# Optimization experiments

Measured on AMD Instinct MI355X. Metric: run time of the kernel, lower is better.

The kernel has to match this reference:

```python
import jax, jax.numpy as jnp
import numpy as np

IN_FEATURES = 4096
OUT_FEATURES = 768
N_BITS = 8
SCALE = float(2 ** N_BITS - 1)  # 255
REG_WEIGHT = 0.001


def setup_inputs() -> dict:
    key = jax.random.key(0)
    k1, k2, k3 = jax.random.split(key, 3)
    latent = jax.random.normal(k1, (1024, IN_FEATURES), dtype=jnp.float32)
    true_sum = jax.random.uniform(k2, (1024, OUT_FEATURES * N_BITS), dtype=jnp.float32)
    # nn.init.uniform_(weight, -0.1, 0.1)
    weight = jax.random.uniform(k3, (IN_FEATURES, OUT_FEATURES * N_BITS),
                                dtype=jnp.float32, minval=-0.1, maxval=0.1)
    return {"latent": latent, "true_sum": true_sum, "weight": weight}


def _powers():
    # [1, 2, 4, ..., 2^(n-1)] with the top (sign) bit negated -> two's complement
    p = 2.0 ** jnp.arange(N_BITS, dtype=jnp.float32)
    return p.at[-1].multiply(-1.0)


def reference(latent, true_sum, weight):
    prob_weights = jax.nn.sigmoid(weight)                      # [in, out*n_bits]
    # min(|p-0|, |p-1|) = min(p, 1-p) for p in (0,1)
    reg_loss = REG_WEIGHT * jnp.minimum(prob_weights, 1.0 - prob_weights).mean()

    powers = _powers()                                         # [n_bits]
    int_weights = jnp.einsum('iob,b->io',
                             prob_weights.reshape(IN_FEATURES, -1, N_BITS),
                             powers)                           # [in, out]
    int_sum = jnp.einsum('nob,b->no',
                         true_sum.reshape(true_sum.shape[0], -1, N_BITS),
                         powers)                               # [B, out]

    # (latent[:, :, None] * int_weights[None]).sum(-2) == latent @ int_weights
    pred = jnp.einsum('bi,io->bo', latent, int_weights)        # [B, out]

    recon_loss = jnp.mean((pred / SCALE - int_sum / SCALE) ** 2)
    return (recon_loss + reg_loss, recon_loss, reg_loss)
```

## Files before the change

### kernel.cpp

```cpp
#include <hip/hip_runtime.h>
#include <hip/hip_bf16.h>
#include <stdint.h>

#define IN_F   4096
#define OUT_F  768
#define OUTB   (OUT_F * 8)
#define BATCH  1024
#define SPLITK 4
#define KSPAN  (IN_F / SPLITK)
#define BK     64
#define NIT    (KSPAN / BK)
#define PLANE  (BATCH * OUT_F)
#define PLANE4 (PLANE / 4)
#define EPIBLK 768

typedef short short8  __attribute__((ext_vector_type(8)));
typedef float f32x4   __attribute__((ext_vector_type(4)));
typedef unsigned int u32;

#define WS_WP    12582912
#define WS_LABF  18874368
#define WS_REGP  27262976
#define WS_SQP   27269120

__device__ __forceinline__ ushort f2bf(float f) {
    uint32_t u = __builtin_bit_cast(uint32_t, f);
    u += 0x7FFFu + ((u >> 16) & 1u);
    return (ushort)(u >> 16);
}

__device__ __forceinline__ float waveReduceSum(float v) {
    #pragma unroll
    for (int off = 32; off > 0; off >>= 1) v += __shfl_down(v, off, 64);
    return v;
}

__device__ __forceinline__ void glds16(const void* g, void* l) {
    __builtin_amdgcn_global_load_lds(
        (const __attribute__((address_space(1))) u32*)g,
        (__attribute__((address_space(3))) u32*)l, 16, 0, 0);
}

__global__ __launch_bounds__(256) void k_weights(const float* __restrict__ w,
                                                 const float* __restrict__ latent,
                                                 ushort* __restrict__ wp,
                                                 ushort* __restrict__ labf,
                                                 float* __restrict__ regpart) {
    if (blockIdx.x >= 1536) {
        int t = (blockIdx.x - 1536) * 256 + threadIdx.x;
        const float4* src = (const float4*)latent;
        uint4* dst = (uint4*)labf;
        #pragma unroll
        for (int j = 0; j < 4; j++) {
            int o = j * 131072 + t;
            float4 a0 = src[2 * o];
            float4 a1 = src[2 * o + 1];
            union { ushort u[8]; uint4 v; } pk;
            pk.u[0] = f2bf(a0.x); pk.u[1] = f2bf(a0.y); pk.u[2] = f2bf(a0.z); pk.u[3] = f2bf(a0.w);
            pk.u[4] = f2bf(a1.x); pk.u[5] = f2bf(a1.y); pk.u[6] = f2bf(a1.z); pk.u[7] = f2bf(a1.w);
            dst[o] = pk.v;
        }
        return;
    }

    int t  = blockIdx.x * 256 + threadIdx.x;
    int o  = t % OUT_F;
    int i8 = t / OUT_F;
    const float* src = w + (size_t)(i8 * 8) * OUTB + (size_t)o * 8;

    const float P[8] = {1.f, 2.f, 4.f, 8.f, 16.f, 32.f, 64.f, -128.f};
    float regsum = 0.f;
    union { ushort u[8]; uint4 v; } pk;

    #pragma unroll
    for (int r = 0; r < 8; r++) {
        float4 a = *(const float4*)(src + (size_t)r * OUTB);
        float4 b = *(const float4*)(src + (size_t)r * OUTB + 4);
        float x[8] = {a.x, a.y, a.z, a.w, b.x, b.y, b.z, b.w};
        float iw = 0.f;
        #pragma unroll
        for (int j = 0; j < 8; j++) {
            float p = __builtin_amdgcn_rcpf(1.f + __expf(-x[j]));
            iw += p * P[j];
            regsum += fminf(p, 1.f - p);
        }
        pk.u[r] = f2bf(iw);
    }
    *(uint4*)(wp + ((size_t)i8 * OUT_F + o) * 8) = pk.v;

    float ws = waveReduceSum(regsum);
    __shared__ float red[4];
    int lane = threadIdx.x & 63, wv = threadIdx.x >> 6;
    if (lane == 0) red[wv] = ws;
    __syncthreads();
    if (threadIdx.x == 0) regpart[blockIdx.x] = red[0] + red[1] + red[2] + red[3];
}

__global__ __launch_bounds__(256) void k_gemm(const ushort* __restrict__ labf,
                                              const ushort* __restrict__ wp,
                                              float* __restrict__ predp) {
    __shared__ __align__(16) ushort lA[2][64 * 72];
    __shared__ __align__(16) ushort lB[2][8 * 1032];

    const int tid  = threadIdx.x;
    const int n0   = blockIdx.x * 64;
    const int m0   = blockIdx.y * 64;
    const int bz   = blockIdx.z;
    const int kbase = bz * KSPAN;
    const int kg0   = kbase >> 3;
    const int lane = tid & 63, w = tid >> 6;
    const int wm = w >> 1, wn = w & 1;
    const int quad = lane >> 4, l16 = lane & 15;

    f32x4 acc[2][2] = {{{0.f,0.f,0.f,0.f},{0.f,0.f,0.f,0.f}},
                       {{0.f,0.f,0.f,0.f},{0.f,0.f,0.f,0.f}}};

    const int ar = tid >> 2, ac = tid & 3;
    const ushort* aptr = labf + (size_t)(m0 + ar) * IN_F + kbase + ac * 16;
    const ushort* bbase = wp + ((size_t)kg0 * OUT_F + n0 + lane) * 8;

    int buf = 0;
    glds16(bbase + (size_t)(2 * w) * OUT_F * 8,     &lB[0][(2 * w) * 1032]);
    glds16(bbase + (size_t)(2 * w + 1) * OUT_F * 8, &lB[0][(2 * w + 1) * 1032]);
    {
        uint4 a0 = *(const uint4*)aptr;
        uint4 a1 = *(const uint4*)(aptr + 8);
        *(uint4*)&lA[0][ar * 72 + ac * 16]     = a0;
        *(uint4*)&lA[0][ar * 72 + ac * 16 + 8] = a1;
    }
    __syncthreads();

    for (int it = 0; it < NIT; ++it) {
        const int nxt = buf ^ 1;
        uint4 a0, a1;
        if (it + 1 < NIT) {
            const ushort* bp = bbase + (size_t)(it + 1) * 8 * OUT_F * 8;
            glds16(bp + (size_t)(2 * w) * OUT_F * 8,     &lB[nxt][(2 * w) * 1032]);
            glds16(bp + (size_t)(2 * w + 1) * OUT_F * 8, &lB[nxt][(2 * w + 1) * 1032]);
            a0 = *(const uint4*)(aptr + (it + 1) * BK);
            a1 = *(const uint4*)(aptr + (it + 1) * BK + 8);
        }
        #pragma unroll
        for (int s = 0; s < 2; ++s) {
            short8 af0 = *(short8*)&lA[buf][(wm * 32 + l16) * 72 + s * 32 + quad * 8];
            short8 af1 = *(short8*)&lA[buf][(wm * 32 + 16 + l16) * 72 + s * 32 + quad * 8];
            short8 bf0 = *(short8*)&lB[buf][(s * 4 + quad) * 1032 + (wn * 32 + l16) * 8];
            short8 bf1 = *(short8*)&lB[buf][(s * 4 + quad) * 1032 + (wn * 32 + 16 + l16) * 8];
            acc[0][0] = __builtin_amdgcn_mfma_f32_16x16x32_bf16(af0, bf0, acc[0][0], 0, 0, 0);
            acc[0][1] = __builtin_amdgcn_mfma_f32_16x16x32_bf16(af0, bf1, acc[0][1], 0, 0, 0);
            acc[1][0] = __builtin_amdgcn_mfma_f32_16x16x32_bf16(af1, bf0, acc[1][0], 0, 0, 0);
            acc[1][1] = __builtin_amdgcn_mfma_f32_16x16x32_bf16(af1, bf1, acc[1][1], 0, 0, 0);
        }
        if (it + 1 < NIT) {
            *(uint4*)&lA[nxt][ar * 72 + ac * 16]     = a0;
            *(uint4*)&lA[nxt][ar * 72 + ac * 16 + 8] = a1;
        }
        __syncthreads();
        buf = nxt;
    }

    float* plane = predp + (size_t)bz * PLANE;
    #pragma unroll
    for (int fm = 0; fm < 2; fm++)
    #pragma unroll
    for (int fn = 0; fn < 2; fn++)
    #pragma unroll
    for (int r = 0; r < 4; r++) {
        int m = m0 + wm * 32 + fm * 16 + quad * 4 + r;
        int n = n0 + wn * 32 + fn * 16 + l16;
        plane[(size_t)m * OUT_F + n] = acc[fm][fn][r];
    }
}

__global__ __launch_bounds__(256) void k_epi(const float* __restrict__ predp,
                                             const float* __restrict__ tsum,
                                             float* __restrict__ sqpart) {
    int g = blockIdx.x * 256 + threadIdx.x;
    int m = g / (OUT_F / 4);
    int c = g % (OUT_F / 4);
    const float4* pp = (const float4*)predp;
    float4 p0 = pp[g];
    float4 p1 = pp[g + PLANE4];
    float4 p2 = pp[g + 2 * PLANE4];
    float4 p3 = pp[g + 3 * PLANE4];
    float pv[4] = {p0.x + p1.x + p2.x + p3.x, p0.y + p1.y + p2.y + p3.y,
                   p0.z + p1.z + p2.z + p3.z, p0.w + p1.w + p2.w + p3.w};
    const float* ts = tsum + (size_t)m * OUTB + (size_t)c * 32;
    float lsum = 0.f;
    #pragma unroll
    for (int j = 0; j < 4; j++) {
        float4 t0 = *(const float4*)(ts + j * 8);
        float4 t1 = *(const float4*)(ts + j * 8 + 4);
        float isum = t0.x + 2.f * t0.y + 4.f * t0.z + 8.f * t0.w
                   + 16.f * t1.x + 32.f * t1.y + 64.f * t1.z - 128.f * t1.w;
        float d = pv[j] - isum;
        lsum += d * d;
    }
    float wsum = waveReduceSum(lsum);
    __shared__ float red[4];
    if ((threadIdx.x & 63) == 0) red[threadIdx.x >> 6] = wsum;
    __syncthreads();
    if (threadIdx.x == 0)
        sqpart[blockIdx.x] = red[0] + red[1] + red[2] + red[3];
}

__global__ __launch_bounds__(256) void k_fin(const float* __restrict__ regpart,
                                             const float* __restrict__ sqpart,
                                             float* __restrict__ out) {
    int tid = threadIdx.x;
    float r = 0.f, s = 0.f;
    #pragma unroll
    for (int j = 0; j < 6; j++) r += regpart[tid + j * 256];
    #pragma unroll
    for (int j = 0; j < 3; j++) s += sqpart[tid + j * 256];
    r = waveReduceSum(r);
    s = waveReduceSum(s);
    __shared__ float redR[4], redS[4];
    int lane = tid & 63, wv = tid >> 6;
    if (lane == 0) { redR[wv] = r; redS[wv] = s; }
    __syncthreads();
    if (tid == 0) {
        float R = redR[0] + redR[1] + redR[2] + redR[3];
        float S = redS[0] + redS[1] + redS[2] + redS[3];
        float recon = S / ((float)(BATCH * OUT_F) * 255.f * 255.f);
        float reg   = 0.001f * R / (float)((size_t)IN_F * OUTB);
        out[0] = recon + reg;
        out[1] = recon;
        out[2] = reg;
    }
}

extern "C" void kernel_launch(void* const* d_in, const int* in_sizes, int n_in,
                              void* d_out, int out_size, void* d_ws, size_t ws_size,
                              hipStream_t stream) {
    const float* latent = (const float*)d_in[0];
    const float* tsum   = (const float*)d_in[1];
    const float* weight = (const float*)d_in[2];
    float* out      = (float*)d_out;
    float* predp    = (float*)d_ws;
    ushort* wp      = (ushort*)((char*)d_ws + WS_WP);
    ushort* labf    = (ushort*)((char*)d_ws + WS_LABF);
    float* regpart  = (float*)((char*)d_ws + WS_REGP);
    float* sqpart   = (float*)((char*)d_ws + WS_SQP);

    k_weights<<<2048, 256, 0, stream>>>(weight, latent, wp, labf, regpart);
    k_gemm<<<dim3(OUT_F / 64, BATCH / 64, SPLITK), 256, 0, stream>>>(labf, wp, predp);
    k_epi<<<EPIBLK, 256, 0, stream>>>(predp, tsum, sqpart);
    k_fin<<<1, 256, 0, stream>>>(regpart, sqpart, out);
}
```

Baseline: 201.7 us.

## Fuse GEMM with loss epilogue and final reduction, drop split-K

Removes split-K so each GEMM block accumulates the full K dimension and computes the squared-error loss directly from its accumulators against true_sum, eliminating the partial-prediction planes written and re-read by a separate epilogue kernel. A last-block-done atomic counter performs the final reduction, replacing two kernel launches. Blocks are remapped with a swizzle that groups M tiles for cache reuse. The trade-off is only 192 blocks with long K loops, which may underfill the GPU compared with the 768-block split-K launch.

```diff
diff --git a/kernel.cpp b/kernel.cpp
--- a/kernel.cpp
+++ b/kernel.cpp
@@ -6,22 +6,19 @@
 #define OUT_F  768
 #define OUTB   (OUT_F * 8)
 #define BATCH  1024
-#define SPLITK 4
-#define KSPAN  (IN_F / SPLITK)
 #define BK     64
-#define NIT    (KSPAN / BK)
-#define PLANE  (BATCH * OUT_F)
-#define PLANE4 (PLANE / 4)
-#define EPIBLK 768
+#define NIT    (IN_F / BK)
+#define NBLK_N (OUT_F / 64)
+#define NBLK_M (BATCH / 64)
+#define NBLK   (NBLK_N * NBLK_M)
+
+#define WS_LABF  6291456
+#define WS_REGP  14680064
+#define WS_CTRL  14686208
 
 typedef short short8  __attribute__((ext_vector_type(8)));
 typedef float f32x4   __attribute__((ext_vector_type(4)));
 typedef unsigned int u32;
-
-#define WS_WP    12582912
-#define WS_LABF  18874368
-#define WS_REGP  27262976
-#define WS_SQP   27269120
 
 __device__ __forceinline__ ushort f2bf(float f) {
     uint32_t u = __builtin_bit_cast(uint32_t, f);
@@ -45,7 +42,12 @@
                                                  const float* __restrict__ latent,
                                                  ushort* __restrict__ wp,
                                                  ushort* __restrict__ labf,
-                                                 float* __restrict__ regpart) {
+                                                 float* __restrict__ regpart,
+                                                 float* __restrict__ ctrl) {
+    if (blockIdx.x == 0 && threadIdx.x == 0) {
+        ctrl[0] = 0.f;
+        ((u32*)ctrl)[1] = 0u;
+    }
     if (blockIdx.x >= 1536) {
         int t = (blockIdx.x - 1536) * 256 + threadIdx.x;
         const float4* src = (const float4*)latent;
@@ -96,18 +98,24 @@
     if (threadIdx.x == 0) regpart[blockIdx.x] = red[0] + red[1] + red[2] + red[3];
 }
 
-__global__ __launch_bounds__(256) void k_gemm(const ushort* __restrict__ labf,
-                                              const ushort* __restrict__ wp,
-                                              float* __restrict__ predp) {
+__global__ __launch_bounds__(256) void k_gemm_epi(const ushort* __restrict__ labf,
+                                                  const ushort* __restrict__ wp,
+                                                  const float* __restrict__ tsum,
+                                                  const float* __restrict__ regpart,
+                                                  float* __restrict__ ctrl,
+                                                  float* __restrict__ out) {
     __shared__ __align__(16) ushort lA[2][64 * 72];
     __shared__ __align__(16) ushort lB[2][8 * 1032];
-
-    const int tid  = threadIdx.x;
-    const int n0   = blockIdx.x * 64;
-    const int m0   = blockIdx.y * 64;
-    const int bz   = blockIdx.z;
-    const int kbase = bz * KSPAN;
-    const int kg0   = kbase >> 3;
+    __shared__ float red[4];
+    __shared__ int lastf;
+
+    const int tid = threadIdx.x;
+    const int d  = blockIdx.x;
+    const int xc = d & 7, s = d >> 3;
+    const int gm = xc + 8 * (s / NBLK_N);
+    const int gn = s % NBLK_N;
+    const int n0 = gn * 64;
+    const int m0 = gm * 64;
     const int lane = tid & 63, w = tid >> 6;
     const int wm = w >> 1, wn = w & 1;
     const int quad = lane >> 4, l16 = lane & 15;
@@ -116,8 +124,8 @@
                        {{0.f,0.f,0.f,0.f},{0.f,0.f,0.f,0.f}}};
 
     const int ar = tid >> 2, ac = tid & 3;
-    const ushort* aptr = labf + (size_t)(m0 + ar) * IN_F + kbase + ac * 16;
-    const ushort* bbase = wp + ((size_t)kg0 * OUT_F + n0 + lane) * 8;
+    const ushort* aptr = labf + (size_t)(m0 + ar) * IN_F + ac * 16;
+    const ushort* bbase = wp + (size_t)(n0 + lane) * 8;
 
     int buf = 0;
     glds16(bbase + (size_t)(2 * w) * OUT_F * 8,     &lB[0][(2 * w) * 1032]);
@@ -130,36 +138,37 @@
     }
     __syncthreads();
 
-    for (int it = 0; it < NIT; ++it) {
+    #define MFMA_STEP(B)                                                                  \
+        _Pragma("unroll")                                                                 \
+        for (int ss = 0; ss < 2; ++ss) {                                                  \
+            short8 af0 = *(short8*)&lA[B][(wm * 32 + l16) * 72 + ss * 32 + quad * 8];     \
+            short8 af1 = *(short8*)&lA[B][(wm * 32 + 16 + l16) * 72 + ss * 32 + quad * 8];\
+            short8 bf0 = *(short8*)&lB[B][(ss * 4 + quad) * 1032 + (wn * 32 + l16) * 8];  \
+            short8 bf1 = *(short8*)&lB[B][(ss * 4 + quad) * 1032 + (wn * 32 + 16 + l16) * 8];\
+            acc[0][0] = __builtin_amdgcn_mfma_f32_16x16x32_bf16(af0, bf0, acc[0][0], 0, 0, 0);\
+            acc[0][1] = __builtin_amdgcn_mfma_f32_16x16x32_bf16(af0, bf1, acc[0][1], 0, 0, 0);\
+            acc[1][0] = __builtin_amdgcn_mfma_f32_16x16x32_bf16(af1, bf0, acc[1][0], 0, 0, 0);\
+            acc[1][1] = __builtin_amdgcn_mfma_f32_16x16x32_bf16(af1, bf1, acc[1][1], 0, 0, 0);\
+        }
+
+    #pragma unroll 2
+    for (int it = 0; it < NIT - 1; ++it) {
         const int nxt = buf ^ 1;
-        uint4 a0, a1;
-        if (it + 1 < NIT) {
-            const ushort* bp = bbase + (size_t)(it + 1) * 8 * OUT_F * 8;
-            glds16(bp + (size_t)(2 * w) * OUT_F * 8,     &lB[nxt][(2 * w) * 1032]);
-            glds16(bp + (size_t)(2 * w + 1) * OUT_F * 8, &lB[nxt][(2 * w + 1) * 1032]);
-            a0 = *(const uint4*)(aptr + (it + 1) * BK);
-            a1 = *(const uint4*)(aptr + (it + 1) * BK + 8);
-        }
-        #pragma unroll
-        for (int s = 0; s < 2; ++s) {
-            short8 af0 = *(short8*)&lA[buf][(wm * 32 + l16) * 72 + s * 32 + quad * 8];
-            short8 af1 = *(short8*)&lA[buf][(wm * 32 + 16 + l16) * 72 + s * 32 + quad * 8];
-            short8 bf0 = *(short8*)&lB[buf][(s * 4 + quad) * 1032 + (wn * 32 + l16) * 8];
-            short8 bf1 = *(short8*)&lB[buf][(s * 4 + quad) * 1032 + (wn * 32 + 16 + l16) * 8];
-            acc[0][0] = __builtin_amdgcn_mfma_f32_16x16x32_bf16(af0, bf0, acc[0][0], 0, 0, 0);
-            acc[0][1] = __builtin_amdgcn_mfma_f32_16x16x32_bf16(af0, bf1, acc[0][1], 0, 0, 0);
-            acc[1][0] = __builtin_amdgcn_mfma_f32_16x16x32_bf16(af1, bf0, acc[1][0], 0, 0, 0);
-            acc[1][1] = __builtin_amdgcn_mfma_f32_16x16x32_bf16(af1, bf1, acc[1][1], 0, 0, 0);
-        }
-        if (it + 1 < NIT) {
-            *(uint4*)&lA[nxt][ar * 72 + ac * 16]     = a0;
-            *(uint4*)&lA[nxt][ar * 72 + ac * 16 + 8] = a1;
-        }
+        const ushort* bp = bbase + (size_t)(it + 1) * (8 * OUT_F * 8);
+        glds16(bp + (size_t)(2 * w) * OUT_F * 8,     &lB[nxt][(2 * w) * 1032]);
+        glds16(bp + (size_t)(2 * w + 1) * OUT_F * 8, &lB[nxt][(2 * w + 1) * 1032]);
+        uint4 a0 = *(const uint4*)(aptr + (it + 1) * BK);
+        uint4 a1 = *(const uint4*)(aptr + (it + 1) * BK + 8);
+        MFMA_STEP(buf);
+        *(uint4*)&lA[nxt][ar * 72 + ac * 16]     = a0;
+        *(uint4*)&lA[nxt][ar * 72 + ac * 16 + 8] = a1;
         __syncthreads();
         buf = nxt;
     }
-
-    float* plane = predp + (size_t)bz * PLANE;
+    MFMA_STEP(buf);
+    #undef MFMA_STEP
+
+    float lsum = 0.f;
     #pragma unroll
     for (int fm = 0; fm < 2; fm++)
     #pragma unroll
@@ -168,65 +177,44 @@
     for (int r = 0; r < 4; r++) {
         int m = m0 + wm * 32 + fm * 16 + quad * 4 + r;
         int n = n0 + wn * 32 + fn * 16 + l16;
-        plane[(size_t)m * OUT_F + n] = acc[fm][fn][r];
-    }
-}
-
-__global__ __launch_bounds__(256) void k_epi(const float* __restrict__ predp,
-                                             const float* __restrict__ tsum,
-                                             float* __restrict__ sqpart) {
-    int g = blockIdx.x * 256 + threadIdx.x;
-    int m = g / (OUT_F / 4);
-    int c = g % (OUT_F / 4);
-    const float4* pp = (const float4*)predp;
-    float4 p0 = pp[g];
-    float4 p1 = pp[g + PLANE4];
-    float4 p2 = pp[g + 2 * PLANE4];
-    float4 p3 = pp[g + 3 * PLANE4];
-    float pv[4] = {p0.x + p1.x + p2.x + p3.x, p0.y + p1.y + p2.y + p3.y,
-                   p0.z + p1.z + p2.z + p3.z, p0.w + p1.w + p2.w + p3.w};
-    const float* ts = tsum + (size_t)m * OUTB + (size_t)c * 32;
-    float lsum = 0.f;
-    #pragma unroll
-    for (int j = 0; j < 4; j++) {
-        float4 t0 = *(const float4*)(ts + j * 8);
-        float4 t1 = *(const float4*)(ts + j * 8 + 4);
+        const float* ts = tsum + (size_t)m * OUTB + (size_t)n * 8;
+        float4 t0 = *(const float4*)ts;
+        float4 t1 = *(const float4*)(ts + 4);
         float isum = t0.x + 2.f * t0.y + 4.f * t0.z + 8.f * t0.w
                    + 16.f * t1.x + 32.f * t1.y + 64.f * t1.z - 128.f * t1.w;
-        float d = pv[j] - isum;
-        lsum += d * d;
+        float dv = acc[fm][fn][r] - isum;
+        lsum += dv * dv;
     }
     float wsum = waveReduceSum(lsum);
-    __shared__ float red[4];
-    if ((threadIdx.x & 63) == 0) red[threadIdx.x >> 6] = wsum;
-    __syncthreads();
-    if (threadIdx.x == 0)
-        sqpart[blockIdx.x] = red[0] + red[1] + red[2] + red[3];
-}
-
-__global__ __launch_bounds__(256) void k_fin(const float* __restrict__ regpart,
-                                             const float* __restrict__ sqpart,
-                                             float* __restrict__ out) {
-    int tid = threadIdx.x;
-    float r = 0.f, s = 0.f;
-    #pragma unroll
-    for (int j = 0; j < 6; j++) r += regpart[tid + j * 256];
-    #pragma unroll
-    for (int j = 0; j < 3; j++) s += sqpart[tid + j * 256];
-    r = waveReduceSum(r);
-    s = waveReduceSum(s);
-    __shared__ float redR[4], redS[4];
-    int lane = tid & 63, wv = tid >> 6;
-    if (lane == 0) { redR[wv] = r; redS[wv] = s; }
+    const int lane63 = tid & 63, wv = tid >> 6;
+    if (lane63 == 0) red[wv] = wsum;
     __syncthreads();
     if (tid == 0) {
-        float R = redR[0] + redR[1] + redR[2] + redR[3];
-        float S = redS[0] + redS[1] + redS[2] + redS[3];
-        float recon = S / ((float)(BATCH * OUT_F) * 255.f * 255.f);
-        float reg   = 0.001f * R / (float)((size_t)IN_F * OUTB);
-        out[0] = recon + reg;
-        out[1] = recon;
-        out[2] = reg;
+        float bsum = red[0] + red[1] + red[2] + red[3];
+        atomicAdd(&ctrl[0], bsum);
+        __threadfence();
+        u32 old = atomicAdd(&((u32*)ctrl)[1], 1u);
+        lastf = (old == (u32)(NBLK - 1));
+    }
+    __syncthreads();
+
+    if (lastf) {
+        float r = 0.f;
+        #pragma unroll
+        for (int j = 0; j < 6; j++) r += regpart[tid + j * 256];
+        r = waveReduceSum(r);
+        __syncthreads();
+        if (lane63 == 0) red[wv] = r;
+        __syncthreads();
+        if (tid == 0) {
+            float S = atomicAdd(&ctrl[0], 0.0f);
+            float R = red[0] + red[1] + red[2] + red[3];
+            float recon = S / ((float)(BATCH * OUT_F) * 255.f * 255.f);
+            float reg   = 0.001f * R / (float)((size_t)IN_F * OUTB);
+            out[0] = recon + reg;
+            out[1] = recon;
+            out[2] = reg;
+        }
     }
 }
 
@@ -237,14 +225,11 @@
     const float* tsum   = (const float*)d_in[1];
     const float* weight = (const float*)d_in[2];
     float* out      = (float*)d_out;
-    float* predp    = (float*)d_ws;
-    ushort* wp      = (ushort*)((char*)d_ws + WS_WP);
+    ushort* wp      = (ushort*)d_ws;
     ushort* labf    = (ushort*)((char*)d_ws + WS_LABF);
     float* regpart  = (float*)((char*)d_ws + WS_REGP);
-    float* sqpart   = (float*)((char*)d_ws + WS_SQP);
-
-    k_weights<<<2048, 256, 0, stream>>>(weight, latent, wp, labf, regpart);
-    k_gemm<<<dim3(OUT_F / 64, BATCH / 64, SPLITK), 256, 0, stream>>>(labf, wp, predp);
-    k_epi<<<EPIBLK, 256, 0, stream>>>(predp, tsum, sqpart);
-    k_fin<<<1, 256, 0, stream>>>(regpart, sqpart, out);
-}
+    float* ctrl     = (float*)((char*)d_ws + WS_CTRL);
+
+    k_weights<<<2048, 256, 0, stream>>>(weight, latent, wp, labf, regpart, ctrl);
+    k_gemm_epi<<<NBLK, 256, 0, stream>>>(labf, wp, tsum, regpart, ctrl, out);
+}
```

After: 222.2 us. 1.1x slower.

## Fuse split-K reduction, loss epilogue and final reduce into GEMM via atomic tickets

Applied to the files above, without the earlier changes.

The separate epilogue and finalize kernels are folded into the GEMM. The last split-K block to finish each output tile, detected with a per-tile atomic counter, sums the four partial planes and computes the squared error against true_sum. A global atomic counter then lets the last tile compute the final losses. This removes two kernel launches and their dependency gaps, at the cost of atomics, memory fences and a serialized tail on the last blocks.

```diff
diff --git a/kernel.cpp b/kernel.cpp
--- a/kernel.cpp
+++ b/kernel.cpp
@@ -12,16 +12,17 @@
 #define NIT    (KSPAN / BK)
 #define PLANE  (BATCH * OUT_F)
 #define PLANE4 (PLANE / 4)
-#define EPIBLK 768
+#define NTILE  192
+
+#define WS_WP    12582912
+#define WS_LABF  18874368
+#define WS_REGP  27262976
+#define WS_TICK  27269120
+#define WS_CTRL  27269888
 
 typedef short short8  __attribute__((ext_vector_type(8)));
 typedef float f32x4   __attribute__((ext_vector_type(4)));
 typedef unsigned int u32;
-
-#define WS_WP    12582912
-#define WS_LABF  18874368
-#define WS_REGP  27262976
-#define WS_SQP   27269120
 
 __device__ __forceinline__ ushort f2bf(float f) {
     uint32_t u = __builtin_bit_cast(uint32_t, f);
@@ -45,7 +46,14 @@
                                                  const float* __restrict__ latent,
                                                  ushort* __restrict__ wp,
                                                  ushort* __restrict__ labf,
-                                                 float* __restrict__ regpart) {
+                                                 float* __restrict__ regpart,
+                                                 u32* __restrict__ tiletick,
+                                                 float* __restrict__ ctrl) {
+    if (blockIdx.x == 0) {
+        if (threadIdx.x < NTILE) tiletick[threadIdx.x] = 0u;
+        if (threadIdx.x == NTILE)     ctrl[0] = 0.f;
+        if (threadIdx.x == NTILE + 1) ((u32*)ctrl)[1] = 0u;
+    }
     if (blockIdx.x >= 1536) {
         int t = (blockIdx.x - 1536) * 256 + threadIdx.x;
         const float4* src = (const float4*)latent;
@@ -96,11 +104,18 @@
     if (threadIdx.x == 0) regpart[blockIdx.x] = red[0] + red[1] + red[2] + red[3];
 }
 
-__global__ __launch_bounds__(256) void k_gemm(const ushort* __restrict__ labf,
-                                              const ushort* __restrict__ wp,
-                                              float* __restrict__ predp) {
+__global__ __launch_bounds__(256) void k_gemm_epi(const ushort* __restrict__ labf,
+                                                  const ushort* __restrict__ wp,
+                                                  const float* __restrict__ tsum,
+                                                  const float* __restrict__ regpart,
+                                                  float* __restrict__ predp,
+                                                  u32* __restrict__ tiletick,
+                                                  float* __restrict__ ctrl,
+                                                  float* __restrict__ out) {
     __shared__ __align__(16) ushort lA[2][64 * 72];
     __shared__ __align__(16) ushort lB[2][8 * 1032];
+    __shared__ float red[4];
+    __shared__ int lastf;
 
     const int tid  = threadIdx.x;
     const int n0   = blockIdx.x * 64;
@@ -170,63 +185,77 @@
         int n = n0 + wn * 32 + fn * 16 + l16;
         plane[(size_t)m * OUT_F + n] = acc[fm][fn][r];
     }
-}
-
-__global__ __launch_bounds__(256) void k_epi(const float* __restrict__ predp,
-                                             const float* __restrict__ tsum,
-                                             float* __restrict__ sqpart) {
-    int g = blockIdx.x * 256 + threadIdx.x;
-    int m = g / (OUT_F / 4);
-    int c = g % (OUT_F / 4);
+
+    __threadfence();
+    __syncthreads();
+    const int tile_id = blockIdx.y * 12 + blockIdx.x;
+    u32 told = 0;
+    if (tid == 0) {
+        told = __hip_atomic_fetch_add(&tiletick[tile_id], 1u,
+                                      __ATOMIC_ACQ_REL, __HIP_MEMORY_SCOPE_AGENT);
+        lastf = (told == (u32)(SPLITK - 1));
+    }
+    __syncthreads();
+    if (!lastf) return;
+    __threadfence();
+
+    const int r16 = tid >> 4, c16 = tid & 15;
     const float4* pp = (const float4*)predp;
-    float4 p0 = pp[g];
-    float4 p1 = pp[g + PLANE4];
-    float4 p2 = pp[g + 2 * PLANE4];
-    float4 p3 = pp[g + 3 * PLANE4];
-    float pv[4] = {p0.x + p1.x + p2.x + p3.x, p0.y + p1.y + p2.y + p3.y,
-                   p0.z + p1.z + p2.z + p3.z, p0.w + p1.w + p2.w + p3.w};
-    const float* ts = tsum + (size_t)m * OUTB + (size_t)c * 32;
     float lsum = 0.f;
     #pragma unroll
     for (int j = 0; j < 4; j++) {
-        float4 t0 = *(const float4*)(ts + j * 8);
-        float4 t1 = *(const float4*)(ts + j * 8 + 4);
-        float isum = t0.x + 2.f * t0.y + 4.f * t0.z + 8.f * t0.w
-                   + 16.f * t1.x + 32.f * t1.y + 64.f * t1.z - 128.f * t1.w;
-        float d = pv[j] - isum;
-        lsum += d * d;
+        int m = m0 + j * 16 + r16;
+        int n = n0 + c16 * 4;
+        int g = (m * OUT_F + n) >> 2;
+        float4 p0 = pp[g];
+        float4 p1 = pp[g + PLANE4];
+        float4 p2 = pp[g + 2 * PLANE4];
+        float4 p3 = pp[g + 3 * PLANE4];
+        float pv[4] = {p0.x + p1.x + p2.x + p3.x, p0.y + p1.y + p2.y + p3.y,
+                       p0.z + p1.z + p2.z + p3.z, p0.w + p1.w + p2.w + p3.w};
+        const float* ts = tsum + (size_t)m * OUTB + (size_t)n * 8;
+        #pragma unroll
+        for (int q = 0; q < 4; q++) {
+            float4 t0 = *(const float4*)(ts + q * 8);
+            float4 t1 = *(const float4*)(ts + q * 8 + 4);
+            float isum = t0.x + 2.f * t0.y + 4.f * t0.z + 8.f * t0.w
+                       + 16.f * t1.x + 32.f * t1.y + 64.f * t1.z - 128.f * t1.w;
+            float d = pv[q] - isum;
+            lsum += d * d;
+        }
     }
     float wsum = waveReduceSum(lsum);
-    __shared__ float red[4];
-    if ((threadIdx.x & 63) == 0) red[threadIdx.x >> 6] = wsum;
-    __syncthreads();
-    if (threadIdx.x == 0)
-        sqpart[blockIdx.x] = red[0] + red[1] + red[2] + red[3];
-}
-
-__global__ __launch_bounds__(256) void k_fin(const float* __restrict__ regpart,
-                                             const float* __restrict__ sqpart,
-                                             float* __restrict__ out) {
-    int tid = threadIdx.x;
-    float r = 0.f, s = 0.f;
-    #pragma unroll
-    for (int j = 0; j < 6; j++) r += regpart[tid + j * 256];
-    #pragma unroll
-    for (int j = 0; j < 3; j++) s += sqpart[tid + j * 256];
-    r = waveReduceSum(r);
-    s = waveReduceSum(s);
-    __shared__ float redR[4], redS[4];
-    int lane = tid & 63, wv = tid >> 6;
-    if (lane == 0) { redR[wv] = r; redS[wv] = s; }
+    const int wv = tid >> 6;
+    if ((tid & 63) == 0) red[wv] = wsum;
     __syncthreads();
     if (tid == 0) {
-        float R = redR[0] + redR[1] + redR[2] + redR[3];
-        float S = redS[0] + redS[1] + redS[2] + redS[3];
-        float recon = S / ((float)(BATCH * OUT_F) * 255.f * 255.f);
-        float reg   = 0.001f * R / (float)((size_t)IN_F * OUTB);
-        out[0] = recon + reg;
-        out[1] = recon;
-        out[2] = reg;
+        float bsum = red[0] + red[1] + red[2] + red[3];
+        atomicAdd(&ctrl[0], bsum);
+        __threadfence();
+        u32 gold = __hip_atomic_fetch_add(&((u32*)ctrl)[1], 1u,
+                                          __ATOMIC_ACQ_REL, __HIP_MEMORY_SCOPE_AGENT);
+        lastf = (gold == (u32)(NTILE - 1));
+    }
+    __syncthreads();
+
+    if (lastf) {
+        __threadfence();
+        float r = 0.f;
+        #pragma unroll
+        for (int j = 0; j < 6; j++) r += regpart[tid + j * 256];
+        r = waveReduceSum(r);
+        __syncthreads();
+        if ((tid & 63) == 0) red[wv] = r;
+        __syncthreads();
+        if (tid == 0) {
+            float S = atomicAdd(&ctrl[0], 0.0f);
+            float R = red[0] + red[1] + red[2] + red[3];
+            float recon = S / ((float)(BATCH * OUT_F) * 255.f * 255.f);
+            float reg   = 0.001f * R / (float)((size_t)IN_F * OUTB);
+            out[0] = recon + reg;
+            out[1] = recon;
+            out[2] = reg;
+        }
     }
 }
 
@@ -241,10 +270,10 @@
     ushort* wp      = (ushort*)((char*)d_ws + WS_WP);
     ushort* labf    = (ushort*)((char*)d_ws + WS_LABF);
     float* regpart  = (float*)((char*)d_ws + WS_REGP);
-    float* sqpart   = (float*)((char*)d_ws + WS_SQP);
-
-    k_weights<<<2048, 256, 0, stream>>>(weight, latent, wp, labf, regpart);
-    k_gemm<<<dim3(OUT_F / 64, BATCH / 64, SPLITK), 256, 0, stream>>>(labf, wp, predp);
-    k_epi<<<EPIBLK, 256, 0, stream>>>(predp, tsum, sqpart);
-    k_fin<<<1, 256, 0, stream>>>(regpart, sqpart, out);
-}
+    u32*   tiletick = (u32*)((char*)d_ws + WS_TICK);
+    float* ctrl     = (float*)((char*)d_ws + WS_CTRL);
+
+    k_weights<<<2048, 256, 0, stream>>>(weight, latent, wp, labf, regpart, tiletick, ctrl);
+    k_gemm_epi<<<dim3(OUT_F / 64, BATCH / 64, SPLITK), 256, 0, stream>>>(
+        labf, wp, tsum, regpart, predp, tiletick, ctrl, out);
+}
```

Result: slower. 344.3 us (+70.7%).

## Enlarge GEMM M-tile to 128, double split-K, fuse final reduction via last-block atomics

Applied to the files above, without the earlier changes.

The GEMM tile grows from 64x64 to 128x64, with each wave computing 32x64, so every B fragment read from shared memory feeds more MFMAs. Split-K doubles to 8 to keep the grid size similar, which doubles the partial-sum planes the epilogue must read. The separate finalize kernel is removed: each epilogue block atomically adds its squared-error sum, and the last block to arrive computes the outputs. The atomic float accumulation makes the order of summation nondeterministic, and the larger tile raises register and LDS use.

```diff
diff --git a/kernel.cpp b/kernel.cpp
--- a/kernel.cpp
+++ b/kernel.cpp
@@ -6,7 +6,7 @@
 #define OUT_F  768
 #define OUTB   (OUT_F * 8)
 #define BATCH  1024
-#define SPLITK 4
+#define SPLITK 8
 #define KSPAN  (IN_F / SPLITK)
 #define BK     64
 #define NIT    (KSPAN / BK)
@@ -14,14 +14,14 @@
 #define PLANE4 (PLANE / 4)
 #define EPIBLK 768
 
+#define WS_WP    25165824
+#define WS_LABF  31457280
+#define WS_REGP  39845888
+#define WS_CTRL  39852032
+
 typedef short short8  __attribute__((ext_vector_type(8)));
 typedef float f32x4   __attribute__((ext_vector_type(4)));
 typedef unsigned int u32;
-
-#define WS_WP    12582912
-#define WS_LABF  18874368
-#define WS_REGP  27262976
-#define WS_SQP   27269120
 
 __device__ __forceinline__ ushort f2bf(float f) {
     uint32_t u = __builtin_bit_cast(uint32_t, f);
@@ -45,7 +45,12 @@
                                                  const float* __restrict__ latent,
                                                  ushort* __restrict__ wp,
                                                  ushort* __restrict__ labf,
-                                                 float* __restrict__ regpart) {
+                                                 float* __restrict__ regpart,
+                                                 float* __restrict__ ctrl) {
+    if (blockIdx.x == 0 && threadIdx.x == 0) {
+        ctrl[0] = 0.f;
+        ((u32*)ctrl)[1] = 0u;
+    }
     if (blockIdx.x >= 1536) {
         int t = (blockIdx.x - 1536) * 256 + threadIdx.x;
         const float4* src = (const float4*)latent;
@@ -99,24 +104,23 @@
 __global__ __launch_bounds__(256) void k_gemm(const ushort* __restrict__ labf,
                                               const ushort* __restrict__ wp,
                                               float* __restrict__ predp) {
-    __shared__ __align__(16) ushort lA[2][64 * 72];
+    __shared__ __align__(16) ushort lA[2][128 * 72];
     __shared__ __align__(16) ushort lB[2][8 * 1032];
 
     const int tid  = threadIdx.x;
     const int n0   = blockIdx.x * 64;
-    const int m0   = blockIdx.y * 64;
+    const int m0   = blockIdx.y * 128;
     const int bz   = blockIdx.z;
     const int kbase = bz * KSPAN;
     const int kg0   = kbase >> 3;
     const int lane = tid & 63, w = tid >> 6;
-    const int wm = w >> 1, wn = w & 1;
     const int quad = lane >> 4, l16 = lane & 15;
 
-    f32x4 acc[2][2] = {{{0.f,0.f,0.f,0.f},{0.f,0.f,0.f,0.f}},
-                       {{0.f,0.f,0.f,0.f},{0.f,0.f,0.f,0.f}}};
-
-    const int ar = tid >> 2, ac = tid & 3;
-    const ushort* aptr = labf + (size_t)(m0 + ar) * IN_F + kbase + ac * 16;
+    f32x4 acc[2][4] = {{{0.f,0.f,0.f,0.f},{0.f,0.f,0.f,0.f},{0.f,0.f,0.f,0.f},{0.f,0.f,0.f,0.f}},
+                       {{0.f,0.f,0.f,0.f},{0.f,0.f,0.f,0.f},{0.f,0.f,0.f,0.f},{0.f,0.f,0.f,0.f}}};
+
+    const int ar = tid >> 1, ac = tid & 1;
+    const ushort* aptr = labf + (size_t)(m0 + ar) * IN_F + kbase + ac * 32;
     const ushort* bbase = wp + ((size_t)kg0 * OUT_F + n0 + lane) * 8;
 
     int buf = 0;
@@ -125,35 +129,50 @@
     {
         uint4 a0 = *(const uint4*)aptr;
         uint4 a1 = *(const uint4*)(aptr + 8);
-        *(uint4*)&lA[0][ar * 72 + ac * 16]     = a0;
-        *(uint4*)&lA[0][ar * 72 + ac * 16 + 8] = a1;
+        uint4 a2 = *(const uint4*)(aptr + 16);
+        uint4 a3 = *(const uint4*)(aptr + 24);
+        *(uint4*)&lA[0][ar * 72 + ac * 32]      = a0;
+        *(uint4*)&lA[0][ar * 72 + ac * 32 + 8]  = a1;
+        *(uint4*)&lA[0][ar * 72 + ac * 32 + 16] = a2;
+        *(uint4*)&lA[0][ar * 72 + ac * 32 + 24] = a3;
     }
     __syncthreads();
 
     for (int it = 0; it < NIT; ++it) {
         const int nxt = buf ^ 1;
-        uint4 a0, a1;
+        uint4 a0, a1, a2, a3;
         if (it + 1 < NIT) {
             const ushort* bp = bbase + (size_t)(it + 1) * 8 * OUT_F * 8;
             glds16(bp + (size_t)(2 * w) * OUT_F * 8,     &lB[nxt][(2 * w) * 1032]);
             glds16(bp + (size_t)(2 * w + 1) * OUT_F * 8, &lB[nxt][(2 * w + 1) * 1032]);
-            a0 = *(const uint4*)(aptr + (it + 1) * BK);
-            a1 = *(const uint4*)(aptr + (it + 1) * BK + 8);
+            const ushort* ap = aptr + (it + 1) * BK;
+            a0 = *(const uint4*)ap;
+            a1 = *(const uint4*)(ap + 8);
+            a2 = *(const uint4*)(ap + 16);
+            a3 = *(const uint4*)(ap + 24);
         }
         #pragma unroll
         for (int s = 0; s < 2; ++s) {
-            short8 af0 = *(short8*)&lA[buf][(wm * 32 + l16) * 72 + s * 32 + quad * 8];
-            short8 af1 = *(short8*)&lA[buf][(wm * 32 + 16 + l16) * 72 + s * 32 + quad * 8];
-            short8 bf0 = *(short8*)&lB[buf][(s * 4 + quad) * 1032 + (wn * 32 + l16) * 8];
-            short8 bf1 = *(short8*)&lB[buf][(s * 4 + quad) * 1032 + (wn * 32 + 16 + l16) * 8];
-            acc[0][0] = __builtin_amdgcn_mfma_f32_16x16x32_bf16(af0, bf0, acc[0][0], 0, 0, 0);
-            acc[0][1] = __builtin_amdgcn_mfma_f32_16x16x32_bf16(af0, bf1, acc[0][1], 0, 0, 0);
-            acc[1][0] = __builtin_amdgcn_mfma_f32_16x16x32_bf16(af1, bf0, acc[1][0], 0, 0, 0);
-            acc[1][1] = __builtin_amdgcn_mfma_f32_16x16x32_bf16(af1, bf1, acc[1][1], 0, 0, 0);
+            short8 af0 = *(short8*)&lA[buf][(w * 32 + l16) * 72 + s * 32 + quad * 8];
+            short8 af1 = *(short8*)&lA[buf][(w * 32 + 16 + l16) * 72 + s * 32 + quad * 8];
+            short8 bq0 = *(short8*)&lB[buf][(s * 4 + quad) * 1032 + l16 * 8];
+            short8 bq1 = *(short8*)&lB[buf][(s * 4 + quad) * 1032 + (16 + l16) * 8];
+            short8 bq2 = *(short8*)&lB[buf][(s * 4 + quad) * 1032 + (32 + l16) * 8];
+            short8 bq3 = *(short8*)&lB[buf][(s * 4 + quad) * 1032 + (48 + l16) * 8];
+            acc[0][0] = __builtin_amdgcn_mfma_f32_16x16x32_bf16(af0, bq0, acc[0][0], 0, 0, 0);
+            acc[0][1] = __builtin_amdgcn_mfma_f32_16x16x32_bf16(af0, bq1, acc[0][1], 0, 0, 0);
+            acc[0][2] = __builtin_amdgcn_mfma_f32_16x16x32_bf16(af0, bq2, acc[0][2], 0, 0, 0);
+            acc[0][3] = __builtin_amdgcn_mfma_f32_16x16x32_bf16(af0, bq3, acc[0][3], 0, 0, 0);
+            acc[1][0] = __builtin_amdgcn_mfma_f32_16x16x32_bf16(af1, bq0, acc[1][0], 0, 0, 0);
+            acc[1][1] = __builtin_amdgcn_mfma_f32_16x16x32_bf16(af1, bq1, acc[1][1], 0, 0, 0);
+            acc[1][2] = __builtin_amdgcn_mfma_f32_16x16x32_bf16(af1, bq2, acc[1][2], 0, 0, 0);
+            acc[1][3] = __builtin_amdgcn_mfma_f32_16x16x32_bf16(af1, bq3, acc[1][3], 0, 0, 0);
         }
         if (it + 1 < NIT) {
-            *(uint4*)&lA[nxt][ar * 72 + ac * 16]     = a0;
-            *(uint4*)&lA[nxt][ar * 72 + ac * 16 + 8] = a1;
+            *(uint4*)&lA[nxt][ar * 72 + ac * 32]      = a0;
+            *(uint4*)&lA[nxt][ar * 72 + ac * 32 + 8]  = a1;
+            *(uint4*)&lA[nxt][ar * 72 + ac * 32 + 16] = a2;
+            *(uint4*)&lA[nxt][ar * 72 + ac * 32 + 24] = a3;
         }
         __syncthreads();
         buf = nxt;
@@ -163,28 +182,30 @@
     #pragma unroll
     for (int fm = 0; fm < 2; fm++)
     #pragma unroll
-    for (int fn = 0; fn < 2; fn++)
+    for (int fn = 0; fn < 4; fn++)
     #pragma unroll
     for (int r = 0; r < 4; r++) {
-        int m = m0 + wm * 32 + fm * 16 + quad * 4 + r;
-        int n = n0 + wn * 32 + fn * 16 + l16;
+        int m = m0 + w * 32 + fm * 16 + quad * 4 + r;
+        int n = n0 + fn * 16 + l16;
         plane[(size_t)m * OUT_F + n] = acc[fm][fn][r];
     }
 }
 
 __global__ __launch_bounds__(256) void k_epi(const float* __restrict__ predp,
                                              const float* __restrict__ tsum,
-                                             float* __restrict__ sqpart) {
+                                             const float* __restrict__ regpart,
+                                             float* __restrict__ ctrl,
+                                             float* __restrict__ out) {
     int g = blockIdx.x * 256 + threadIdx.x;
     int m = g / (OUT_F / 4);
     int c = g % (OUT_F / 4);
     const float4* pp = (const float4*)predp;
-    float4 p0 = pp[g];
-    float4 p1 = pp[g + PLANE4];
-    float4 p2 = pp[g + 2 * PLANE4];
-    float4 p3 = pp[g + 3 * PLANE4];
-    float pv[4] = {p0.x + p1.x + p2.x + p3.x, p0.y + p1.y + p2.y + p3.y,
-                   p0.z + p1.z + p2.z + p3.z, p0.w + p1.w + p2.w + p3.w};
+    float pv[4] = {0.f, 0.f, 0.f, 0.f};
+    #pragma unroll
+    for (int p = 0; p < SPLITK; p++) {
+        float4 q = pp[g + p * PLANE4];
+        pv[0] += q.x; pv[1] += q.y; pv[2] += q.z; pv[3] += q.w;
+    }
     const float* ts = tsum + (size_t)m * OUTB + (size_t)c * 32;
     float lsum = 0.f;
     #pragma unroll
@@ -198,30 +219,28 @@
     }
     float wsum = waveReduceSum(lsum);
     __shared__ float red[4];
-    if ((threadIdx.x & 63) == 0) red[threadIdx.x >> 6] = wsum;
-    __syncthreads();
-    if (threadIdx.x == 0)
-        sqpart[blockIdx.x] = red[0] + red[1] + red[2] + red[3];
-}
-
-__global__ __launch_bounds__(256) void k_fin(const float* __restrict__ regpart,
-                                             const float* __restrict__ sqpart,
-                                             float* __restrict__ out) {
-    int tid = threadIdx.x;
-    float r = 0.f, s = 0.f;
-    #pragma unroll
-    for (int j = 0; j < 6; j++) r += regpart[tid + j * 256];
-    #pragma unroll
-    for (int j = 0; j < 3; j++) s += sqpart[tid + j * 256];
+    __shared__ int lastf;
+    int lane = threadIdx.x & 63, wv = threadIdx.x >> 6;
+    if (lane == 0) red[wv] = wsum;
+    __syncthreads();
+    if (threadIdx.x == 0) {
+        atomicAdd(&ctrl[0], red[0] + red[1] + red[2] + red[3]);
+        u32 t = __hip_atomic_fetch_add((u32*)ctrl + 1, 1u,
+                                       __ATOMIC_RELEASE, __HIP_MEMORY_SCOPE_AGENT);
+        lastf = (t == (u32)(EPIBLK - 1));
+    }
+    __syncthreads();
+    if (!lastf) return;
+
+    float r = 0.f;
+    #pragma unroll
+    for (int j = 0; j < 6; j++) r += regpart[threadIdx.x + j * 256];
     r = waveReduceSum(r);
-    s = waveReduceSum(s);
-    __shared__ float redR[4], redS[4];
-    int lane = tid & 63, wv = tid >> 6;
-    if (lane == 0) { redR[wv] = r; redS[wv] = s; }
-    __syncthreads();
-    if (tid == 0) {
-        float R = redR[0] + redR[1] + redR[2] + redR[3];
-        float S = redS[0] + redS[1] + redS[2] + redS[3];
+    if (lane == 0) red[wv] = r;
+    __syncthreads();
+    if (threadIdx.x == 0) {
+        float S = atomicAdd(&ctrl[0], 0.0f);
+        float R = red[0] + red[1] + red[2] + red[3];
         float recon = S / ((float)(BATCH * OUT_F) * 255.f * 255.f);
         float reg   = 0.001f * R / (float)((size_t)IN_F * OUTB);
         out[0] = recon + reg;
@@ -241,10 +260,9 @@
     ushort* wp      = (ushort*)((char*)d_ws + WS_WP);
     ushort* labf    = (ushort*)((char*)d_ws + WS_LABF);
     float* regpart  = (float*)((char*)d_ws + WS_REGP);
-    float* sqpart   = (float*)((char*)d_ws + WS_SQP);
-
-    k_weights<<<2048, 256, 0, stream>>>(weight, latent, wp, labf, regpart);
-    k_gemm<<<dim3(OUT_F / 64, BATCH / 64, SPLITK), 256, 0, stream>>>(labf, wp, predp);
-    k_epi<<<EPIBLK, 256, 0, stream>>>(predp, tsum, sqpart);
-    k_fin<<<1, 256, 0, stream>>>(regpart, sqpart, out);
-}
+    float* ctrl     = (float*)((char*)d_ws + WS_CTRL);
+
+    k_weights<<<2048, 256, 0, stream>>>(weight, latent, wp, labf, regpart, ctrl);
+    k_gemm<<<dim3(OUT_F / 64, BATCH / 128, SPLITK), 256, 0, stream>>>(labf, wp, predp);
+    k_epi<<<EPIBLK, 256, 0, stream>>>(predp, tsum, regpart, ctrl, out);
+}
```

After: 231.5 us. +14.7%, slower.
